# Kernel optimization log

Hardware: AMD Instinct MI355X
Metric: run time of the kernel (lower is better)

Reference implementation:

```python
import jax, jax.numpy as jnp
import numpy as np

CLAMP = 1e20
EPS_LN = 1e-5
EPS_DEN = 1e-5


def setup_inputs() -> dict:
    key = jax.random.key(0)
    ks = jax.random.split(key, 8)
    B, T, Fin, D = 4, 2048, 512, 128
    s = 1.0 / np.sqrt(Fin)
    s2 = 1.0 / np.sqrt(D)
    return {
        "history": jax.random.normal(ks[0], (B, T, Fin), dtype=jnp.float32),
        "S0": jnp.zeros((B, 1, D, D), dtype=jnp.float32),
        "Z0": jnp.zeros((B, 1, D), dtype=jnp.float32),
        "Wk": jax.random.normal(ks[1], (Fin, D), dtype=jnp.float32) * s,
        "Wq": jax.random.normal(ks[2], (Fin, D), dtype=jnp.float32) * s,
        "Wv": jax.random.normal(ks[3], (Fin, D), dtype=jnp.float32) * s,
        "ln_g": jnp.ones((Fin,), dtype=jnp.float32),
        "ln_b": jnp.zeros((Fin,), dtype=jnp.float32),
        "w1": jax.random.normal(ks[4], (D, D), dtype=jnp.float32) * s2,
        "b1": jnp.zeros((D,), dtype=jnp.float32),
        "w2": jax.random.normal(ks[5], (D, D), dtype=jnp.float32) * s2,
        "b2": jnp.zeros((D,), dtype=jnp.float32),
        "sc_w": jax.random.normal(ks[6], (Fin, D), dtype=jnp.float32) * s,
        "sc_b": jnp.zeros((D,), dtype=jnp.float32),
    }


def reference(history, S0, Z0, Wk, Wq, Wv, ln_g, ln_b, w1, b1, w2, b2, sc_w, sc_b):
    # LayerNorm over feature dim
    mu = jnp.mean(history, axis=-1, keepdims=True)
    var = jnp.mean((history - mu) ** 2, axis=-1, keepdims=True)
    x = (history - mu) / jnp.sqrt(var + EPS_LN) * ln_g + ln_b  # [B,T,Fin]

    phi = lambda z: jax.nn.elu(z) + 1.0
    K = phi(x @ Wk)  # [B,T,D]
    Q = phi(x @ Wq)  # [B,T,D]
    V = x @ Wv       # [B,T,D]

    # S_t = clamp(cumsum_t(K_t outer V_t)) + S0  -> [B,T,D,D]
    KV = jnp.einsum('bti,btj->btij', K, V)
    S = jnp.clip(jnp.cumsum(KV, axis=1), -CLAMP, CLAMP) + S0
    # Z_t = clamp(cumsum_t(K_t)) + Z0 -> [B,T,D]
    Z = jnp.clip(jnp.cumsum(K, axis=1), -CLAMP, CLAMP) + Z0

    numerator = jnp.einsum('bti,btil->btl', Q, S)            # [B,T,D]
    denominator = jnp.einsum('bti,bti->bt', Q, Z)[..., None] + EPS_DEN
    out = numerator / denominator

    # feed-forward: Linear->ReLU->Linear->ReLU
    out = jax.nn.relu(jax.nn.relu(out @ w1 + b1) @ w2 + b2)
    # residual shortcut from normalized input
    out = out + x @ sc_w + sc_b
    return out, S, Z
```

## Files before the change

### kernel.cpp

```cpp
#include <hip/hip_runtime.h>
#include <math.h>

#define BB 4
#define TT 2048
#define FIN 512
#define DD 128
#define NC 32
#define CT 64
#define ROWS (BB*TT)
#define CLAMP_V 1e20f
#define EPS_LN_ 1e-5f
#define EPS_DEN_ 1e-5f

__global__ __launch_bounds__(256) void k0_stats(const float* __restrict__ h,
                                                float* __restrict__ stats) {
  int wv = threadIdx.x >> 6, lane = threadIdx.x & 63;
  int row = blockIdx.x * 4 + wv;
  const float* hr = h + (size_t)row * FIN;
  float s = 0.f, sq = 0.f;
#pragma unroll
  for (int j = 0; j < FIN / 64; ++j) {
    float v = hr[lane + 64 * j];
    s += v; sq += v * v;
  }
#pragma unroll
  for (int m = 32; m >= 1; m >>= 1) {
    s += __shfl_xor(s, m);
    sq += __shfl_xor(sq, m);
  }
  if (lane == 0) {
    float mu = s * (1.f / FIN);
    float var = sq * (1.f / FIN) - mu * mu;
    stats[row * 2] = mu;
    stats[row * 2 + 1] = rsqrtf(var + EPS_LN_);
  }
}

__global__ __launch_bounds__(256) void k1_lngemm(
    const float* __restrict__ h, const float* __restrict__ stats,
    const float* __restrict__ ln_g, const float* __restrict__ ln_b,
    const float* __restrict__ Wk, const float* __restrict__ Wq,
    const float* __restrict__ Wv, const float* __restrict__ Wsc,
    float* __restrict__ Kb, float* __restrict__ Qb,
    float* __restrict__ Vb, float* __restrict__ SCb) {
  __shared__ float As[32 * 129];
  __shared__ float Bs[32 * 128];
  int tid = threadIdx.x;
  int row0 = blockIdx.x * 128;
  int wsel = blockIdx.y;
  const float* W = (wsel == 0) ? Wk : (wsel == 1) ? Wq : (wsel == 2) ? Wv : Wsc;
  float* Ob = (wsel == 0) ? Kb : (wsel == 1) ? Qb : (wsel == 2) ? Vb : SCb;
  int ty = tid >> 4, tx = tid & 15;
  float acc[8][8];
#pragma unroll
  for (int i = 0; i < 8; ++i)
#pragma unroll
    for (int j = 0; j < 8; ++j) acc[i][j] = 0.f;

  for (int ks = 0; ks < FIN; ks += 32) {
#pragma unroll
    for (int j = 0; j < 16; ++j) {
      int idx = tid + 256 * j;
      int r = idx >> 5, f = idx & 31;
      float v = h[(size_t)(row0 + r) * FIN + ks + f];
      float mu = stats[(row0 + r) * 2], rs = stats[(row0 + r) * 2 + 1];
      As[f * 129 + r] = (v - mu) * rs * ln_g[ks + f] + ln_b[ks + f];
    }
#pragma unroll
    for (int j = 0; j < 16; ++j) {
      int idx = tid + 256 * j;
      int k = idx >> 7, n = idx & 127;
      Bs[k * 128 + n] = W[(size_t)(ks + k) * DD + n];
    }
    __syncthreads();
#pragma unroll
    for (int k = 0; k < 32; ++k) {
      float a[8], bv[8];
#pragma unroll
      for (int i = 0; i < 8; ++i) a[i] = As[k * 129 + ty * 8 + i];
#pragma unroll
      for (int j = 0; j < 8; ++j) bv[j] = Bs[k * 128 + tx * 8 + j];
#pragma unroll
      for (int i = 0; i < 8; ++i)
#pragma unroll
        for (int j = 0; j < 8; ++j) acc[i][j] = fmaf(a[i], bv[j], acc[i][j]);
    }
    __syncthreads();
  }
  bool phi = (wsel < 2);
#pragma unroll
  for (int i = 0; i < 8; ++i) {
    int row = row0 + ty * 8 + i;
#pragma unroll
    for (int j = 0; j < 8; ++j) {
      float z = acc[i][j];
      if (phi) z = (z > 0.f) ? (z + 1.f) : expf(z);
      Ob[(size_t)row * DD + tx * 8 + j] = z;
    }
  }
}

__global__ __launch_bounds__(256) void k2_chunksum(const float* __restrict__ Kb,
                                                   const float* __restrict__ Vb,
                                                   float* __restrict__ kvsum,
                                                   float* __restrict__ ksum) {
  int bc = blockIdx.x;
  int b = bc >> 5, c = bc & 31;
  __shared__ float Kc[CT * 128];
  __shared__ float Vc[CT * 128];
  int tid = threadIdx.x;
  size_t base = (size_t)(b * TT + c * CT) * 128;
#pragma unroll
  for (int j = 0; j < 32; ++j) {
    int idx = tid + 256 * j;
    Kc[idx] = Kb[base + idx];
    Vc[idx] = Vb[base + idx];
  }
  __syncthreads();
  int ti = tid >> 4, tl = tid & 15;
  int i0 = ti * 8, l0 = tl * 8;
  float acc[8][8];
#pragma unroll
  for (int i = 0; i < 8; ++i)
#pragma unroll
    for (int j = 0; j < 8; ++j) acc[i][j] = 0.f;
  for (int t = 0; t < CT; ++t) {
    float kk[8], vv[8];
#pragma unroll
    for (int i = 0; i < 8; ++i) kk[i] = Kc[t * 128 + i0 + i];
#pragma unroll
    for (int j = 0; j < 8; ++j) vv[j] = Vc[t * 128 + l0 + j];
#pragma unroll
    for (int i = 0; i < 8; ++i)
#pragma unroll
      for (int j = 0; j < 8; ++j) acc[i][j] = fmaf(kk[i], vv[j], acc[i][j]);
  }
  size_t ob = (size_t)bc * 16384;
#pragma unroll
  for (int i = 0; i < 8; ++i)
#pragma unroll
    for (int j = 0; j < 8; ++j)
      kvsum[ob + (size_t)(i0 + i) * 128 + l0 + j] = acc[i][j];
  if (tid < 128) {
    float s = 0.f;
    for (int t = 0; t < CT; ++t) s += Kc[t * 128 + tid];
    ksum[bc * 128 + tid] = s;
  }
}

__global__ __launch_bounds__(256) void k3_prefix(float* __restrict__ kvsum) {
  int gid = blockIdx.x * 256 + threadIdx.x;
  int b = gid >> 14, rem = gid & 16383;
  size_t base = (size_t)b * NC * 16384 + rem;
  float run = 0.f;
  for (int c = 0; c < NC; ++c) {
    size_t idx = base + (size_t)c * 16384;
    float t = kvsum[idx];
    kvsum[idx] = run;
    run += t;
  }
}

__global__ __launch_bounds__(128) void k4_z(const float* __restrict__ Kb,
                                            const float* __restrict__ ksum,
                                            const float* __restrict__ Z0,
                                            float* __restrict__ Zout) {
  int bc = blockIdx.x; int b = bc >> 5, c = bc & 31;
  int i = threadIdx.x;
  float z = 0.f;
  for (int cc = 0; cc < c; ++cc) z += ksum[(b * NC + cc) * 128 + i];
  float z0 = Z0[b * 128 + i];
#pragma unroll 4
  for (int t = 0; t < CT; ++t) {
    int gt = c * CT + t;
    z += Kb[(size_t)(b * TT + gt) * 128 + i];
    float zc = fminf(fmaxf(z, -CLAMP_V), CLAMP_V) + z0;
    Zout[(size_t)(b * TT + gt) * 128 + i] = zc;
  }
}

__global__ __launch_bounds__(256) void k5_den(const float* __restrict__ Qb,
                                              const float* __restrict__ Zout,
                                              float* __restrict__ den) {
  int wv = threadIdx.x >> 6, lane = threadIdx.x & 63;
  int row = blockIdx.x * 4 + wv;
  size_t o = (size_t)row * 128;
  float p = Qb[o + lane] * Zout[o + lane] + Qb[o + 64 + lane] * Zout[o + 64 + lane];
#pragma unroll
  for (int m = 32; m >= 1; m >>= 1) p += __shfl_xor(p, m);
  if (lane == 0) den[row] = p + EPS_DEN_;
}

__global__ __launch_bounds__(256) void k6_main(
    const float* __restrict__ Kb, const float* __restrict__ Qb,
    const float* __restrict__ Vb, const float* __restrict__ kvpref,
    const float* __restrict__ S0, float* __restrict__ Sout,
    float* __restrict__ numpart) {
  __shared__ float KQ[CT * 128 * 2];
  int tid = threadIdx.x;
  int lhalf = blockIdx.x, c = blockIdx.y, b = blockIdx.z;
  int w = tid >> 6, lane = tid & 63;
  int i0 = w * 32;
  int l = lhalf * 64 + lane;
  size_t rowbase = (size_t)(b * TT + c * CT) * 128;
#pragma unroll
  for (int j = 0; j < 32; ++j) {
    int idx = tid + 256 * j;
    KQ[idx * 2] = Kb[rowbase + idx];
    KQ[idx * 2 + 1] = Qb[rowbase + idx];
  }
  float s[32], s0[32];
  int bc = b * NC + c;
#pragma unroll
  for (int ii = 0; ii < 32; ++ii) {
    s[ii] = kvpref[(size_t)bc * 16384 + (size_t)(i0 + ii) * 128 + l];
    s0[ii] = S0[((size_t)b * 128 + i0 + ii) * 128 + l];
  }
  __syncthreads();
  for (int t = 0; t < CT; ++t) {
    int gt = c * CT + t;
    float v = Vb[(size_t)(b * TT + gt) * 128 + l];
    float num = 0.f;
    size_t sb = ((size_t)(b * TT + gt) * 128 + i0) * 128 + l;
#pragma unroll
    for (int ii = 0; ii < 32; ++ii) {
      float2 kq = *(const float2*)&KQ[(t * 128 + i0 + ii) * 2];
      s[ii] = fmaf(kq.x, v, s[ii]);
      float sc = fminf(fmaxf(s[ii], -CLAMP_V), CLAMP_V) + s0[ii];
      __builtin_nontemporal_store(sc, &Sout[sb + (size_t)ii * 128]);
      num = fmaf(kq.y, sc, num);
    }
    numpart[(size_t)w * ROWS * 128 + (size_t)(b * TT + gt) * 128 + l] = num;
  }
}

__global__ __launch_bounds__(256) void k7_ff(
    const float* __restrict__ numpart, const float* __restrict__ den,
    const float* __restrict__ w1, const float* __restrict__ b1,
    const float* __restrict__ w2, const float* __restrict__ b2,
    const float* __restrict__ SCb, const float* __restrict__ sc_b,
    float* __restrict__ out) {
  __shared__ float a[64 * 128];
  __shared__ float h1[64 * 128];
  int tid = threadIdx.x;
  int row0 = blockIdx.x * 64;
#pragma unroll
  for (int j = 0; j < 32; ++j) {
    int idx = tid + 256 * j;
    int r = idx >> 7;
    size_t g = (size_t)(row0 + r) * 128 + (idx & 127);
    float s = numpart[g] + numpart[g + (size_t)ROWS * 128] +
              numpart[g + 2 * (size_t)ROWS * 128] + numpart[g + 3 * (size_t)ROWS * 128];
    a[idx] = s / den[row0 + r];
  }
  __syncthreads();
  int l = tid & 127, half = tid >> 7;
  for (int rc = 0; rc < 4; ++rc) {
    int r0 = half * 32 + rc * 8;
    float acc[8];
#pragma unroll
    for (int rr = 0; rr < 8; ++rr) acc[rr] = b1[l];
    for (int k = 0; k < 128; ++k) {
      float wv = w1[k * 128 + l];
#pragma unroll
      for (int rr = 0; rr < 8; ++rr) acc[rr] = fmaf(a[(r0 + rr) * 128 + k], wv, acc[rr]);
    }
#pragma unroll
    for (int rr = 0; rr < 8; ++rr) h1[(r0 + rr) * 128 + l] = fmaxf(acc[rr], 0.f);
  }
  __syncthreads();
  for (int rc = 0; rc < 4; ++rc) {
    int r0 = half * 32 + rc * 8;
    float acc[8];
#pragma unroll
    for (int rr = 0; rr < 8; ++rr) acc[rr] = b2[l];
    for (int k = 0; k < 128; ++k) {
      float wv = w2[k * 128 + l];
#pragma unroll
      for (int rr = 0; rr < 8; ++rr) acc[rr] = fmaf(h1[(r0 + rr) * 128 + k], wv, acc[rr]);
    }
#pragma unroll
    for (int rr = 0; rr < 8; ++rr) {
      int row = row0 + r0 + rr;
      out[(size_t)row * 128 + l] =
          fmaxf(acc[rr], 0.f) + SCb[(size_t)row * 128 + l] + sc_b[l];
    }
  }
}

extern "C" void kernel_launch(void* const* d_in, const int* in_sizes, int n_in,
                              void* d_out, int out_size, void* d_ws, size_t ws_size,
                              hipStream_t stream) {
  const float* history = (const float*)d_in[0];
  const float* S0   = (const float*)d_in[1];
  const float* Z0   = (const float*)d_in[2];
  const float* Wk   = (const float*)d_in[3];
  const float* Wq   = (const float*)d_in[4];
  const float* Wv   = (const float*)d_in[5];
  const float* ln_g = (const float*)d_in[6];
  const float* ln_b = (const float*)d_in[7];
  const float* w1   = (const float*)d_in[8];
  const float* b1   = (const float*)d_in[9];
  const float* w2   = (const float*)d_in[10];
  const float* b2   = (const float*)d_in[11];
  const float* sc_w = (const float*)d_in[12];
  const float* sc_b = (const float*)d_in[13];

  float* out  = (float*)d_out;
  float* Sout = out + (size_t)ROWS * DD;
  float* Zout = Sout + (size_t)ROWS * DD * DD;

  float* ws = (float*)d_ws;
  float* stats   = ws;
  float* Kb      = stats + 16384;
  float* Qb      = Kb + (size_t)ROWS * DD;
  float* Vb      = Qb + (size_t)ROWS * DD;
  float* SCb     = Vb + (size_t)ROWS * DD;
  float* kvsum   = SCb + (size_t)ROWS * DD;
  float* ksum    = kvsum + (size_t)BB * NC * 16384;
  float* numpart = ksum + BB * NC * 128;
  float* den     = numpart + 4 * (size_t)ROWS * DD;

  k0_stats<<<ROWS / 4, 256, 0, stream>>>(history, stats);
  k1_lngemm<<<dim3(ROWS / 128, 4), 256, 0, stream>>>(history, stats, ln_g, ln_b,
                                                     Wk, Wq, Wv, sc_w,
                                                     Kb, Qb, Vb, SCb);
  k2_chunksum<<<BB * NC, 256, 0, stream>>>(Kb, Vb, kvsum, ksum);
  k3_prefix<<<(BB * DD * DD) / 256, 256, 0, stream>>>(kvsum);
  k4_z<<<BB * NC, 128, 0, stream>>>(Kb, ksum, Z0, Zout);
  k5_den<<<ROWS / 4, 256, 0, stream>>>(Qb, Zout, den);
  k6_main<<<dim3(2, NC, BB), 256, 0, stream>>>(Kb, Qb, Vb, kvsum, S0, Sout, numpart);
  k7_ff<<<ROWS / 64, 256, 0, stream>>>(numpart, den, w1, b1, w2, b2, SCb, sc_b, out);
}
```

Baseline: 752.7 us.

## Halve chunk size, prefetch GEMM tiles, fuse Z/den and numerator reduction

Halves the chunk length so the S-writing kernel launches twice as many blocks. It adds register prefetching of the next LayerNorm/weight tile in the projection GEMM and caches LN params and stats in shared memory. The Z prefix, denominator and ksum prefix are fused into the existing kernels, and the four numerator partials are reduced in shared memory instead of going through a global buffer. The FF kernel then reads a single normalized attention buffer with smaller tiles. This costs more chunk-summary traffic (kvsum doubles) and extra shared memory in the main kernel.

Result: no change. 739.3 us (-1.8%).

```diff
diff --git a/kernel.cpp b/kernel.cpp
--- a/kernel.cpp
+++ b/kernel.cpp
@@ -5,8 +5,8 @@
 #define TT 2048
 #define FIN 512
 #define DD 128
-#define NC 32
-#define CT 64
+#define NC 64
+#define CT 32
 #define ROWS (BB*TT)
 #define CLAMP_V 1e20f
 #define EPS_LN_ 1e-5f
@@ -45,34 +45,55 @@
     float* __restrict__ Vb, float* __restrict__ SCb) {
   __shared__ float As[32 * 129];
   __shared__ float Bs[32 * 128];
+  __shared__ float stS[256];
+  __shared__ float lnS[2 * FIN];
   int tid = threadIdx.x;
   int row0 = blockIdx.x * 128;
   int wsel = blockIdx.y;
   const float* W = (wsel == 0) ? Wk : (wsel == 1) ? Wq : (wsel == 2) ? Wv : Wsc;
   float* Ob = (wsel == 0) ? Kb : (wsel == 1) ? Qb : (wsel == 2) ? Vb : SCb;
   int ty = tid >> 4, tx = tid & 15;
+  if (tid < 128) {
+    stS[tid * 2] = stats[(row0 + tid) * 2];
+    stS[tid * 2 + 1] = stats[(row0 + tid) * 2 + 1];
+  }
+  for (int j = tid; j < FIN; j += 256) {
+    lnS[j] = ln_g[j];
+    lnS[FIN + j] = ln_b[j];
+  }
   float acc[8][8];
 #pragma unroll
   for (int i = 0; i < 8; ++i)
 #pragma unroll
     for (int j = 0; j < 8; ++j) acc[i][j] = 0.f;
 
+  int ar = tid >> 5, af = tid & 31;
+  int bk = tid >> 7, bn = tid & 127;
+  float ra[16], rb[16];
+#pragma unroll
+  for (int j = 0; j < 16; ++j) {
+    ra[j] = h[(size_t)(row0 + ar + 8 * j) * FIN + af];
+    rb[j] = W[(size_t)(bk + 2 * j) * DD + bn];
+  }
+  __syncthreads();
+#pragma unroll
+  for (int j = 0; j < 16; ++j) {
+    int r = ar + 8 * j;
+    float mu = stS[r * 2], rs = stS[r * 2 + 1];
+    As[af * 129 + r] = (ra[j] - mu) * rs * lnS[af] + lnS[FIN + af];
+    Bs[(bk + 2 * j) * 128 + bn] = rb[j];
+  }
+  __syncthreads();
+
   for (int ks = 0; ks < FIN; ks += 32) {
-#pragma unroll
-    for (int j = 0; j < 16; ++j) {
-      int idx = tid + 256 * j;
-      int r = idx >> 5, f = idx & 31;
-      float v = h[(size_t)(row0 + r) * FIN + ks + f];
-      float mu = stats[(row0 + r) * 2], rs = stats[(row0 + r) * 2 + 1];
-      As[f * 129 + r] = (v - mu) * rs * ln_g[ks + f] + ln_b[ks + f];
-    }
-#pragma unroll
-    for (int j = 0; j < 16; ++j) {
-      int idx = tid + 256 * j;
-      int k = idx >> 7, n = idx & 127;
-      Bs[k * 128 + n] = W[(size_t)(ks + k) * DD + n];
-    }
-    __syncthreads();
+    bool more = (ks + 32) < FIN;
+    if (more) {
+#pragma unroll
+      for (int j = 0; j < 16; ++j) {
+        ra[j] = h[(size_t)(row0 + ar + 8 * j) * FIN + ks + 32 + af];
+        rb[j] = W[(size_t)(ks + 32 + bk + 2 * j) * DD + bn];
+      }
+    }
 #pragma unroll
     for (int k = 0; k < 32; ++k) {
       float a[8], bv[8];
@@ -86,6 +107,16 @@
         for (int j = 0; j < 8; ++j) acc[i][j] = fmaf(a[i], bv[j], acc[i][j]);
     }
     __syncthreads();
+    if (more) {
+#pragma unroll
+      for (int j = 0; j < 16; ++j) {
+        int r = ar + 8 * j;
+        float mu = stS[r * 2], rs = stS[r * 2 + 1];
+        As[af * 129 + r] = (ra[j] - mu) * rs * lnS[ks + 32 + af] + lnS[FIN + ks + 32 + af];
+        Bs[(bk + 2 * j) * 128 + bn] = rb[j];
+      }
+      __syncthreads();
+    }
   }
   bool phi = (wsel < 2);
 #pragma unroll
@@ -105,13 +136,13 @@
                                                    float* __restrict__ kvsum,
                                                    float* __restrict__ ksum) {
   int bc = blockIdx.x;
-  int b = bc >> 5, c = bc & 31;
+  int b = bc >> 6, c = bc & 63;
   __shared__ float Kc[CT * 128];
   __shared__ float Vc[CT * 128];
   int tid = threadIdx.x;
   size_t base = (size_t)(b * TT + c * CT) * 128;
 #pragma unroll
-  for (int j = 0; j < 32; ++j) {
+  for (int j = 0; j < 16; ++j) {
     int idx = tid + 256 * j;
     Kc[idx] = Kb[base + idx];
     Vc[idx] = Vb[base + idx];
@@ -148,7 +179,8 @@
   }
 }
 
-__global__ __launch_bounds__(256) void k3_prefix(float* __restrict__ kvsum) {
+__global__ __launch_bounds__(256) void k3_prefix(float* __restrict__ kvsum,
+                                                 float* __restrict__ ksum) {
   int gid = blockIdx.x * 256 + threadIdx.x;
   int b = gid >> 14, rem = gid & 16383;
   size_t base = (size_t)b * NC * 16384 + rem;
@@ -159,52 +191,68 @@
     kvsum[idx] = run;
     run += t;
   }
-}
-
-__global__ __launch_bounds__(128) void k4_z(const float* __restrict__ Kb,
-                                            const float* __restrict__ ksum,
-                                            const float* __restrict__ Z0,
-                                            float* __restrict__ Zout) {
-  int bc = blockIdx.x; int b = bc >> 5, c = bc & 31;
+  if (gid < BB * 128) {
+    int b2 = gid >> 7, i = gid & 127;
+    float r2 = 0.f;
+    for (int c = 0; c < NC; ++c) {
+      int idx = (b2 * NC + c) * 128 + i;
+      float t = ksum[idx];
+      ksum[idx] = r2;
+      r2 += t;
+    }
+  }
+}
+
+__global__ __launch_bounds__(128) void k4_zden(const float* __restrict__ Kb,
+                                               const float* __restrict__ Qb,
+                                               const float* __restrict__ ksum,
+                                               const float* __restrict__ Z0,
+                                               float* __restrict__ Zout,
+                                               float* __restrict__ den) {
+  __shared__ float denp[2 * CT];
+  int bx = blockIdx.x;
+  int b = bx >> 6, c = bx & 63;
   int i = threadIdx.x;
-  float z = 0.f;
-  for (int cc = 0; cc < c; ++cc) z += ksum[(b * NC + cc) * 128 + i];
+  int wv = i >> 6, lane = i & 63;
+  float z = ksum[(b * NC + c) * 128 + i];
   float z0 = Z0[b * 128 + i];
-#pragma unroll 4
+  size_t rb = (size_t)(b * TT + c * CT) * 128;
+  float kcur = Kb[rb + i], qcur = Qb[rb + i];
   for (int t = 0; t < CT; ++t) {
-    int gt = c * CT + t;
-    z += Kb[(size_t)(b * TT + gt) * 128 + i];
+    float kn = 0.f, qn = 0.f;
+    if (t + 1 < CT) {
+      kn = Kb[rb + (size_t)(t + 1) * 128 + i];
+      qn = Qb[rb + (size_t)(t + 1) * 128 + i];
+    }
+    z += kcur;
     float zc = fminf(fmaxf(z, -CLAMP_V), CLAMP_V) + z0;
-    Zout[(size_t)(b * TT + gt) * 128 + i] = zc;
-  }
-}
-
-__global__ __launch_bounds__(256) void k5_den(const float* __restrict__ Qb,
-                                              const float* __restrict__ Zout,
-                                              float* __restrict__ den) {
-  int wv = threadIdx.x >> 6, lane = threadIdx.x & 63;
-  int row = blockIdx.x * 4 + wv;
-  size_t o = (size_t)row * 128;
-  float p = Qb[o + lane] * Zout[o + lane] + Qb[o + 64 + lane] * Zout[o + 64 + lane];
-#pragma unroll
-  for (int m = 32; m >= 1; m >>= 1) p += __shfl_xor(p, m);
-  if (lane == 0) den[row] = p + EPS_DEN_;
+    Zout[rb + (size_t)t * 128 + i] = zc;
+    float p = qcur * zc;
+#pragma unroll
+    for (int m = 32; m >= 1; m >>= 1) p += __shfl_xor(p, m);
+    if (lane == 0) denp[wv * CT + t] = p;
+    kcur = kn; qcur = qn;
+  }
+  __syncthreads();
+  if (i < CT) den[b * TT + c * CT + i] = denp[i] + denp[CT + i] + EPS_DEN_;
 }
 
 __global__ __launch_bounds__(256) void k6_main(
     const float* __restrict__ Kb, const float* __restrict__ Qb,
     const float* __restrict__ Vb, const float* __restrict__ kvpref,
-    const float* __restrict__ S0, float* __restrict__ Sout,
-    float* __restrict__ numpart) {
+    const float* __restrict__ S0, const float* __restrict__ den,
+    float* __restrict__ Sout, float* __restrict__ Aout) {
   __shared__ float KQ[CT * 128 * 2];
+  __shared__ float NA[4 * CT * 64];
   int tid = threadIdx.x;
   int lhalf = blockIdx.x, c = blockIdx.y, b = blockIdx.z;
   int w = tid >> 6, lane = tid & 63;
   int i0 = w * 32;
   int l = lhalf * 64 + lane;
-  size_t rowbase = (size_t)(b * TT + c * CT) * 128;
-#pragma unroll
-  for (int j = 0; j < 32; ++j) {
+  int row0r = b * TT + c * CT;
+  size_t rowbase = (size_t)row0r * 128;
+#pragma unroll
+  for (int j = 0; j < 16; ++j) {
     int idx = tid + 256 * j;
     KQ[idx * 2] = Kb[rowbase + idx];
     KQ[idx * 2 + 1] = Qb[rowbase + idx];
@@ -217,11 +265,12 @@
     s0[ii] = S0[((size_t)b * 128 + i0 + ii) * 128 + l];
   }
   __syncthreads();
+  float v = Vb[rowbase + l];
   for (int t = 0; t < CT; ++t) {
-    int gt = c * CT + t;
-    float v = Vb[(size_t)(b * TT + gt) * 128 + l];
+    float vn = 0.f;
+    if (t + 1 < CT) vn = Vb[rowbase + (size_t)(t + 1) * 128 + l];
     float num = 0.f;
-    size_t sb = ((size_t)(b * TT + gt) * 128 + i0) * 128 + l;
+    size_t sb = ((size_t)(row0r + t) * 128 + i0) * 128 + l;
 #pragma unroll
     for (int ii = 0; ii < 32; ++ii) {
       float2 kq = *(const float2*)&KQ[(t * 128 + i0 + ii) * 2];
@@ -230,33 +279,40 @@
       __builtin_nontemporal_store(sc, &Sout[sb + (size_t)ii * 128]);
       num = fmaf(kq.y, sc, num);
     }
-    numpart[(size_t)w * ROWS * 128 + (size_t)(b * TT + gt) * 128 + l] = num;
+    NA[(w * CT + t) * 64 + lane] = num;
+    v = vn;
+  }
+  __syncthreads();
+#pragma unroll
+  for (int j = 0; j < 8; ++j) {
+    int idx = tid + 256 * j;
+    int t = idx >> 6, ll = idx & 63;
+    int row = row0r + t;
+    float sum = NA[idx] + NA[CT * 64 + idx] + NA[2 * CT * 64 + idx] +
+                NA[3 * CT * 64 + idx];
+    Aout[(size_t)row * 128 + lhalf * 64 + ll] = sum / den[row];
   }
 }
 
 __global__ __launch_bounds__(256) void k7_ff(
-    const float* __restrict__ numpart, const float* __restrict__ den,
+    const float* __restrict__ A,
     const float* __restrict__ w1, const float* __restrict__ b1,
     const float* __restrict__ w2, const float* __restrict__ b2,
     const float* __restrict__ SCb, const float* __restrict__ sc_b,
     float* __restrict__ out) {
-  __shared__ float a[64 * 128];
-  __shared__ float h1[64 * 128];
+  __shared__ float a[32 * 128];
+  __shared__ float h1[32 * 128];
   int tid = threadIdx.x;
-  int row0 = blockIdx.x * 64;
-#pragma unroll
-  for (int j = 0; j < 32; ++j) {
+  int row0 = blockIdx.x * 32;
+#pragma unroll
+  for (int j = 0; j < 16; ++j) {
     int idx = tid + 256 * j;
-    int r = idx >> 7;
-    size_t g = (size_t)(row0 + r) * 128 + (idx & 127);
-    float s = numpart[g] + numpart[g + (size_t)ROWS * 128] +
-              numpart[g + 2 * (size_t)ROWS * 128] + numpart[g + 3 * (size_t)ROWS * 128];
-    a[idx] = s / den[row0 + r];
+    a[idx] = A[(size_t)(row0 + (idx >> 7)) * 128 + (idx & 127)];
   }
   __syncthreads();
   int l = tid & 127, half = tid >> 7;
-  for (int rc = 0; rc < 4; ++rc) {
-    int r0 = half * 32 + rc * 8;
+  for (int rc = 0; rc < 2; ++rc) {
+    int r0 = half * 16 + rc * 8;
     float acc[8];
 #pragma unroll
     for (int rr = 0; rr < 8; ++rr) acc[rr] = b1[l];
@@ -269,8 +325,8 @@
     for (int rr = 0; rr < 8; ++rr) h1[(r0 + rr) * 128 + l] = fmaxf(acc[rr], 0.f);
   }
   __syncthreads();
-  for (int rc = 0; rc < 4; ++rc) {
-    int r0 = half * 32 + rc * 8;
+  for (int rc = 0; rc < 2; ++rc) {
+    int r0 = half * 16 + rc * 8;
     float acc[8];
 #pragma unroll
     for (int rr = 0; rr < 8; ++rr) acc[rr] = b2[l];
@@ -311,24 +367,23 @@
   float* Zout = Sout + (size_t)ROWS * DD * DD;
 
   float* ws = (float*)d_ws;
-  float* stats   = ws;
-  float* Kb      = stats + 16384;
-  float* Qb      = Kb + (size_t)ROWS * DD;
-  float* Vb      = Qb + (size_t)ROWS * DD;
-  float* SCb     = Vb + (size_t)ROWS * DD;
-  float* kvsum   = SCb + (size_t)ROWS * DD;
-  float* ksum    = kvsum + (size_t)BB * NC * 16384;
-  float* numpart = ksum + BB * NC * 128;
-  float* den     = numpart + 4 * (size_t)ROWS * DD;
+  float* stats = ws;
+  float* Kb    = stats + 16384;
+  float* Qb    = Kb + (size_t)ROWS * DD;
+  float* Vb    = Qb + (size_t)ROWS * DD;
+  float* SCb   = Vb + (size_t)ROWS * DD;
+  float* kvsum = SCb + (size_t)ROWS * DD;
+  float* ksum  = kvsum + (size_t)BB * NC * 16384;
+  float* A     = ksum + (size_t)BB * NC * 128;
+  float* den   = A + (size_t)ROWS * DD;
 
   k0_stats<<<ROWS / 4, 256, 0, stream>>>(history, stats);
   k1_lngemm<<<dim3(ROWS / 128, 4), 256, 0, stream>>>(history, stats, ln_g, ln_b,
                                                      Wk, Wq, Wv, sc_w,
                                                      Kb, Qb, Vb, SCb);
   k2_chunksum<<<BB * NC, 256, 0, stream>>>(Kb, Vb, kvsum, ksum);
-  k3_prefix<<<(BB * DD * DD) / 256, 256, 0, stream>>>(kvsum);
-  k4_z<<<BB * NC, 128, 0, stream>>>(Kb, ksum, Z0, Zout);
-  k5_den<<<ROWS / 4, 256, 0, stream>>>(Qb, Zout, den);
-  k6_main<<<dim3(2, NC, BB), 256, 0, stream>>>(Kb, Qb, Vb, kvsum, S0, Sout, numpart);
-  k7_ff<<<ROWS / 64, 256, 0, stream>>>(numpart, den, w1, b1, w2, b2, SCb, sc_b, out);
-}
+  k3_prefix<<<(BB * DD * DD) / 256, 256, 0, stream>>>(kvsum, ksum);
+  k4_zden<<<BB * NC, 128, 0, stream>>>(Kb, Qb, ksum, Z0, Zout, den);
+  k6_main<<<dim3(2, NC, BB), 256, 0, stream>>>(Kb, Qb, Vb, kvsum, S0, den, Sout, A);
+  k7_ff<<<ROWS / 32, 256, 0, stream>>>(A, w1, b1, w2, b2, SCb, sc_b, out);
+}
```
